# Optimization experiments

Measured on AMD Instinct MI355X. Metric: run time of the kernel, lower is better.

Reference implementation:

```python
import jax, jax.numpy as jnp
import numpy as np

B, T, HW, ENC, DEC, ATT, EMB, V = 32, 128, 14, 2048, 512, 512, 512, 10000
P = HW * HW  # num_pixels = 196


def setup_inputs() -> dict:
    key = jax.random.key(0)
    ks = jax.random.split(key, 24)
    s = 0.02
    inp = {
        'bimgs': jax.random.normal(ks[0], (B, HW, HW, ENC), dtype=jnp.float32),
        'bx': jax.random.randint(ks[1], (B, T), 0, V),
        # torch code assumes lengths sorted DESCENDING
        'bxlen': jnp.sort(jax.random.randint(ks[2], (B,), 1, T + 1))[::-1],
        'emb_W': jax.random.normal(ks[3], (V, EMB)) * s,
        'enc_att_W': jax.random.normal(ks[4], (ATT, ENC)) * s,
        'enc_att_b': jnp.zeros((ATT,)),
        'dec_att_W': jax.random.normal(ks[5], (ATT, DEC)) * s,
        'dec_att_b': jnp.zeros((ATT,)),
        'full_att_W': jax.random.normal(ks[6], (1, ATT)) * s,
        'full_att_b': jnp.zeros((1,)),
        'init_h_W': jax.random.normal(ks[7], (DEC, ENC)) * s,
        'init_h_b': jnp.zeros((DEC,)),
        'init_c_W': jax.random.normal(ks[8], (DEC, ENC)) * s,
        'init_c_b': jnp.zeros((DEC,)),
        'f_beta_W': jax.random.normal(ks[9], (ENC, DEC)) * s,
        'f_beta_b': jnp.zeros((ENC,)),
        'W_ih': jax.random.normal(ks[10], (4 * DEC, EMB + ENC)) * s,
        'b_ih': jnp.zeros((4 * DEC,)),
        'W_hh': jax.random.normal(ks[11], (4 * DEC, DEC)) * s,
        'b_hh': jnp.zeros((4 * DEC,)),
        'fc_W': jax.random.normal(ks[12], (V, DEC)) * s,
        'fc_b': jnp.zeros((V,)),
    }
    return inp


def reference(bimgs, bx, bxlen, emb_W, enc_att_W, enc_att_b, dec_att_W, dec_att_b,
              full_att_W, full_att_b, init_h_W, init_h_b, init_c_W, init_c_b,
              f_beta_W, f_beta_b, W_ih, b_ih, W_hh, b_hh, fc_W, fc_b):
    b = bimgs.shape[0]
    imgs = bimgs.reshape(b, -1, bimgs.shape[-1])          # [B,P,enc]
    t_len = bx.shape[-1]
    embeds = emb_W[bx]                                     # [B,T,E]
    mean_img = imgs.mean(axis=1)                           # [B,enc]
    h0 = mean_img @ init_h_W.T + init_h_b                  # [B,dec]
    c0 = mean_img @ init_c_W.T + init_c_b
    # encoder attention projection is time-invariant -> hoist out of the loop
    att1 = imgs @ enc_att_W.T + enc_att_b                  # [B,P,A]
    active_ts = jnp.arange(t_len)[:, None] < bxlen[None, :]  # [T,B]
    emb_ts = embeds.transpose(1, 0, 2)                     # [T,B,E]

    def step(carry, xs):
        h, c = carry
        emb_t, active = xs
        att2 = h @ dec_att_W.T + dec_att_b                 # [B,A]
        e = jax.nn.relu(att1 + att2[:, None, :]) @ full_att_W[0] + full_att_b[0]  # [B,P]
        alpha = jax.nn.softmax(e, axis=1)
        awe = jnp.einsum('bpe,bp->be', imgs, alpha)        # [B,enc]
        gate = jax.nn.sigmoid(h @ f_beta_W.T + f_beta_b)
        x = jnp.concatenate([emb_t, gate * awe], axis=1)   # [B,E+enc]
        # PyTorch LSTMCell: gate order i, f, g, o
        gates = x @ W_ih.T + b_ih + h @ W_hh.T + b_hh
        i_, f_, g_, o_ = jnp.split(gates, 4, axis=1)
        i_ = jax.nn.sigmoid(i_); f_ = jax.nn.sigmoid(f_); o_ = jax.nn.sigmoid(o_)
        g_ = jnp.tanh(g_)
        c_new = f_ * c + i_ * g_
        h_new = o_ * jnp.tanh(c_new)
        preds = h_new @ fc_W.T + fc_b                      # dropout = identity (eval)
        m = active[:, None]
        h2 = jnp.where(m, h_new, h)
        c2 = jnp.where(m, c_new, c)
        return (h2, c2), (jnp.where(m, preds, 0.0), jnp.where(m, alpha, 0.0))

    _, (preds_ts, alphas_ts) = jax.lax.scan(step, (h0, c0), (emb_ts, active_ts))
    predictions = preds_ts.transpose(1, 0, 2)              # [B,T,V]
    alphas = alphas_ts.transpose(1, 0, 2)                  # [B,T,P]
    return predictions, alphas
```

## Files before the change

### kernel.cpp

```cpp
#include <hip/hip_runtime.h>
#include <hip/hip_bf16.h>

#define BB 32
#define TT 128
#define PP 196
#define ENC 2048
#define DEC 512
#define ATT 512
#define EMB 512
#define VV 10000
#define VVP 10240
#define G4 2048
#define KX 2560

typedef unsigned short u16;
typedef unsigned int u32;
typedef __attribute__((ext_vector_type(8))) short short8;
typedef __attribute__((ext_vector_type(4))) float f32x4;

__device__ __forceinline__ float bf2f(u16 u) { return __uint_as_float(((u32)u) << 16); }
__device__ __forceinline__ u16 f2bf(float f) {
  u32 x = __float_as_uint(f);
  u32 r = (x + 0x7fffu + ((x >> 16) & 1u)) >> 16;
  return (u16)r;
}
__device__ __forceinline__ void unpack8(uint4 v, float* f) {
  f[0] = __uint_as_float(v.x << 16); f[1] = __uint_as_float(v.x & 0xffff0000u);
  f[2] = __uint_as_float(v.y << 16); f[3] = __uint_as_float(v.y & 0xffff0000u);
  f[4] = __uint_as_float(v.z << 16); f[5] = __uint_as_float(v.z & 0xffff0000u);
  f[6] = __uint_as_float(v.w << 16); f[7] = __uint_as_float(v.w & 0xffff0000u);
}
__device__ __forceinline__ void load8(const float* __restrict__ p, float* f) {
  float4 a = ((const float4*)p)[0];
  float4 b = ((const float4*)p)[1];
  f[0] = a.x; f[1] = a.y; f[2] = a.z; f[3] = a.w;
  f[4] = b.x; f[5] = b.y; f[6] = b.z; f[7] = b.w;
}
__device__ __forceinline__ float sigf(float x) { return 1.0f / (1.0f + __expf(-x)); }
__device__ __forceinline__ short8 ld_frag(const u16* __restrict__ p) {
  union { uint4 u; short8 s; } cv;
  cv.u = *(const uint4*)p;
  return cv.s;
}

__global__ __launch_bounds__(256) void k_cvt(const float* __restrict__ src, u16* __restrict__ dst, int n) {
  int i0 = (blockIdx.x * 256 + threadIdx.x) * 8;
  if (i0 >= n) return;
  float f[8]; load8(src + i0, f);
  u16 o[8];
#pragma unroll
  for (int u = 0; u < 8; u++) o[u] = f2bf(f[u]);
  *(uint4*)(dst + i0) = *(const uint4*)o;
}

__global__ __launch_bounds__(256) void k_emball(const int* __restrict__ bx,
    const float* __restrict__ embW, u16* __restrict__ xemb) {
  int flat = blockIdx.x * 256 + threadIdx.x;
  int row = flat >> 6;
  int c8 = (flat & 63) * 8;
  int tok = bx[row];
  const float* e = embW + (size_t)tok * EMB + c8;
  float f[8]; load8(e, f);
  u16 o[8];
#pragma unroll
  for (int u = 0; u < 8; u++) o[u] = f2bf(f[u]);
  *(uint4*)(xemb + (size_t)row * EMB + c8) = *(const uint4*)o;
}

__global__ __launch_bounds__(256) void k_mean(const u16* __restrict__ imgs_bf, u16* __restrict__ mean_bf) {
  int b = blockIdx.x >> 2, chunk = blockIdx.x & 3;
  int ch0 = chunk * 512 + threadIdx.x * 2;
  const u32* base = (const u32*)(imgs_bf + (size_t)b * PP * ENC + ch0);
  float a0 = 0.f, a1 = 0.f;
#pragma unroll 4
  for (int p = 0; p < PP; p++) {
    u32 u = base[(size_t)p * (ENC / 2)];
    a0 += __uint_as_float(u << 16);
    a1 += __uint_as_float(u & 0xffff0000u);
  }
  const float inv = 1.0f / PP;
  u16 o[2] = { f2bf(a0 * inv), f2bf(a1 * inv) };
  *(u32*)(mean_bf + b * ENC + ch0) = *(const u32*)o;
}

__global__ __launch_bounds__(64) void k_init2(const u16* __restrict__ W2_bf,
    const float* __restrict__ ihb, const float* __restrict__ icb,
    const u16* __restrict__ mean_bf, u16* __restrict__ h_bf, float* __restrict__ c) {
  int lane = threadIdx.x;
  int j0 = blockIdx.x * 16;
  int m = lane & 15, quad = lane >> 4;
  const u16* arow = W2_bf + (size_t)(j0 + m) * ENC + quad * 8;
  const u16* xb0 = mean_bf + (size_t)m * ENC + quad * 8;
  const u16* xb1 = mean_bf + (size_t)(16 + m) * ENC + quad * 8;
  f32x4 acc0 = {0.f,0.f,0.f,0.f}, acc1 = {0.f,0.f,0.f,0.f};
  for (int k = 0; k < ENC; k += 32) {
    short8 a = ld_frag(arow + k);
    short8 x0 = ld_frag(xb0 + k);
    short8 x1 = ld_frag(xb1 + k);
    acc0 = __builtin_amdgcn_mfma_f32_16x16x32_bf16(a, x0, acc0, 0, 0, 0);
    acc1 = __builtin_amdgcn_mfma_f32_16x16x32_bf16(a, x1, acc1, 0, 0, 0);
  }
  int jj = j0 + quad * 4;
  int b0 = m, b1 = 16 + m;
#pragma unroll
  for (int r = 0; r < 4; r++) {
    int j = jj + r;
    if (j < 512) {
      float bia = ihb[j];
      h_bf[b0 * DEC + j] = f2bf(acc0[r] + bia);
      h_bf[b1 * DEC + j] = f2bf(acc1[r] + bia);
    } else {
      int g = j - 512;
      float bia = icb[g];
      c[b0 * DEC + g] = acc0[r] + bia;
      c[b1 * DEC + g] = acc1[r] + bia;
    }
  }
}

__global__ __launch_bounds__(256) void k_att1(const u16* __restrict__ imgs_bf,
    const u16* __restrict__ encW_bf, const float* __restrict__ encb, u16* __restrict__ att1) {
  int tid = threadIdx.x;
  int wave = tid >> 6, lane = tid & 63;
  int m0 = blockIdx.x * 32;
  int lm = lane & 15, quad = lane >> 4;
  const u16* b0p = imgs_bf + (size_t)(m0 + lm) * ENC + quad * 8;
  const u16* b1p = imgs_bf + (size_t)(m0 + 16 + lm) * ENC + quad * 8;
  const u16* arow = encW_bf + (size_t)(wave * 128 + lm) * ENC + quad * 8;
  f32x4 acc[8][2];
#pragma unroll
  for (int i = 0; i < 8; i++) { acc[i][0] = (f32x4){0.f,0.f,0.f,0.f}; acc[i][1] = (f32x4){0.f,0.f,0.f,0.f}; }
  for (int k = 0; k < ENC; k += 32) {
    short8 B0 = ld_frag(b0p + k);
    short8 B1 = ld_frag(b1p + k);
#pragma unroll
    for (int i = 0; i < 8; i++) {
      short8 A = ld_frag(arow + (size_t)i * 16 * ENC + k);
      acc[i][0] = __builtin_amdgcn_mfma_f32_16x16x32_bf16(A, B0, acc[i][0], 0, 0, 0);
      acc[i][1] = __builtin_amdgcn_mfma_f32_16x16x32_bf16(A, B1, acc[i][1], 0, 0, 0);
    }
  }
#pragma unroll
  for (int i = 0; i < 8; i++) {
    int jb = wave * 128 + i * 16 + quad * 4;
#pragma unroll
    for (int r = 0; r < 4; r++) {
      int j = jb + r;
      float bia = encb[j];
      att1[(size_t)(m0 + lm) * ATT + j]      = f2bf(acc[i][0][r] + bia);
      att1[(size_t)(m0 + 16 + lm) * ATT + j] = f2bf(acc[i][1][r] + bia);
    }
  }
}

__global__ __launch_bounds__(64) void k_step1(const u16* __restrict__ W3,
    const float* __restrict__ decb, const float* __restrict__ fbb, const float* __restrict__ bhh,
    const u16* __restrict__ h_bf,
    float* __restrict__ att2, float* __restrict__ gate, float* __restrict__ hWhh) {
  int lane = threadIdx.x;
  int j0 = blockIdx.x * 16;
  int m = lane & 15, quad = lane >> 4;
  const u16* arow = W3 + (size_t)(j0 + m) * DEC + quad * 8;
  const u16* xb0 = h_bf + (size_t)m * DEC + quad * 8;
  const u16* xb1 = h_bf + (size_t)(16 + m) * DEC + quad * 8;
  f32x4 acc0 = {0.f,0.f,0.f,0.f}, acc1 = {0.f,0.f,0.f,0.f};
  for (int k = 0; k < DEC; k += 32) {
    short8 a = ld_frag(arow + k);
    short8 x0 = ld_frag(xb0 + k);
    short8 x1 = ld_frag(xb1 + k);
    acc0 = __builtin_amdgcn_mfma_f32_16x16x32_bf16(a, x0, acc0, 0, 0, 0);
    acc1 = __builtin_amdgcn_mfma_f32_16x16x32_bf16(a, x1, acc1, 0, 0, 0);
  }
  int jj = j0 + quad * 4;
  int b0 = m, b1 = 16 + m;
#pragma unroll
  for (int r = 0; r < 4; r++) {
    int j = jj + r;
    float v0 = acc0[r], v1 = acc1[r];
    if (j0 < ATT) {
      float bia = decb[j];
      att2[b0 * ATT + j] = v0 + bia;
      att2[b1 * ATT + j] = v1 + bia;
    } else if (j0 < ATT + ENC) {
      int g = j - ATT;
      float bia = fbb[g];
      gate[b0 * ENC + g] = sigf(v0 + bia);
      gate[b1 * ENC + g] = sigf(v1 + bia);
    } else {
      int g = j - ATT - ENC;
      float bia = bhh[g];
      hWhh[b0 * G4 + g] = v0 + bia;
      hWhh[b1 * G4 + g] = v1 + bia;
    }
  }
}

__global__ __launch_bounds__(256) void k_att(int t, const int* __restrict__ bxlen,
    const u16* __restrict__ att1, const float* __restrict__ att2,
    const float* __restrict__ faW, const float* __restrict__ fab,
    float* __restrict__ alpha_ws, float* __restrict__ out_alphas) {
  int b = blockIdx.x;
  int tid = threadIdx.x;
  if (t >= bxlen[b]) {
    if (tid < PP) out_alphas[((size_t)b * TT + t) * PP + tid] = 0.f;
    return;
  }
  __shared__ float a2[ATT];
  __shared__ float w_s[ATT];
  __shared__ float redw[4], redw2[4];
  for (int i = tid; i < ATT; i += 256) { a2[i] = att2[b * ATT + i]; w_s[i] = faW[i]; }
  __syncthreads();
  float e = -1e30f;
  if (tid < PP) {
    const uint4* ar = (const uint4*)(att1 + (size_t)(b * PP + tid) * ATT);
    float acc = 0.f;
    for (int k = 0; k < ATT; k += 8) {
      float af[8]; unpack8(ar[k >> 3], af);
#pragma unroll
      for (int u = 0; u < 8; u++) {
        float v = af[u] + a2[k + u];
        acc += fmaxf(v, 0.f) * w_s[k + u];
      }
    }
    e = acc + fab[0];
  }
  int lane = tid & 63, wid = tid >> 6;
  float wmax = e;
#pragma unroll
  for (int off = 32; off; off >>= 1) wmax = fmaxf(wmax, __shfl_xor(wmax, off));
  if (lane == 0) redw[wid] = wmax;
  __syncthreads();
  float mx = fmaxf(fmaxf(redw[0], redw[1]), fmaxf(redw[2], redw[3]));
  float ex = (tid < PP) ? __expf(e - mx) : 0.f;
  float wsum = ex;
#pragma unroll
  for (int off = 32; off; off >>= 1) wsum += __shfl_xor(wsum, off);
  if (lane == 0) redw2[wid] = wsum;
  __syncthreads();
  float inv = 1.0f / (redw2[0] + redw2[1] + redw2[2] + redw2[3]);
  if (tid < PP) {
    float al = ex * inv;
    alpha_ws[b * PP + tid] = al;
    out_alphas[((size_t)b * TT + t) * PP + tid] = al;
  }
}

__global__ __launch_bounds__(256) void k_awe(int t, const int* __restrict__ bxlen,
    const u16* __restrict__ imgs_bf, const float* __restrict__ alpha_ws,
    const float* __restrict__ gate, u16* __restrict__ x_awe) {
  int b = blockIdx.x >> 2, chunk = blockIdx.x & 3;
  if (t >= bxlen[b]) return;
  __shared__ float al[PP];
  int tid = threadIdx.x;
  if (tid < PP) al[tid] = alpha_ws[b * PP + tid];
  __syncthreads();
  int ch0 = chunk * 512 + tid * 2;
  const u32* base = (const u32*)(imgs_bf + (size_t)b * PP * ENC + ch0);
  float acc0 = 0.f, acc1 = 0.f;
#pragma unroll 4
  for (int p = 0; p < PP; p++) {
    u32 u = base[(size_t)p * (ENC / 2)];
    float a = al[p];
    acc0 += a * __uint_as_float(u << 16);
    acc1 += a * __uint_as_float(u & 0xffff0000u);
  }
  float2 g = *(const float2*)(gate + b * ENC + ch0);
  u16 o[2] = { f2bf(g.x * acc0), f2bf(g.y * acc1) };
  *(u32*)(x_awe + (size_t)b * ENC + ch0) = *(const u32*)o;
}

__global__ __launch_bounds__(64) void k_gates(int t, const u16* __restrict__ Wih_bf,
    const u16* __restrict__ xemb, const u16* __restrict__ x_awe,
    float* __restrict__ gates_p) {
  int lane = threadIdx.x;
  int j0 = blockIdx.x * 16;
  int y = blockIdx.y;
  int kofs = y * 512;
  int m = lane & 15, quad = lane >> 4;
  const u16* arow = Wih_bf + (size_t)(j0 + m) * KX + kofs + quad * 8;
  const u16 *b0p, *b1p;
  if (y == 0) {
    b0p = xemb + ((size_t)m * TT + t) * EMB + quad * 8;
    b1p = xemb + ((size_t)(16 + m) * TT + t) * EMB + quad * 8;
  } else {
    int ao = kofs - 512;
    b0p = x_awe + (size_t)m * ENC + ao + quad * 8;
    b1p = x_awe + (size_t)(16 + m) * ENC + ao + quad * 8;
  }
  f32x4 acc0 = {0.f,0.f,0.f,0.f}, acc1 = {0.f,0.f,0.f,0.f};
  for (int k = 0; k < 512; k += 32) {
    short8 a = ld_frag(arow + k);
    short8 x0 = ld_frag(b0p + k);
    short8 x1 = ld_frag(b1p + k);
    acc0 = __builtin_amdgcn_mfma_f32_16x16x32_bf16(a, x0, acc0, 0, 0, 0);
    acc1 = __builtin_amdgcn_mfma_f32_16x16x32_bf16(a, x1, acc1, 0, 0, 0);
  }
  float* gp = gates_p + (size_t)y * BB * G4;
  int jj = j0 + quad * 4;
  int b0 = m, b1 = 16 + m;
#pragma unroll
  for (int r = 0; r < 4; r++) {
    int j = jj + r;
    gp[b0 * G4 + j] = acc0[r];
    gp[b1 * G4 + j] = acc1[r];
  }
}

__global__ __launch_bounds__(256) void k_lstm(int t, const int* __restrict__ bxlen,
    const float* __restrict__ gates_p, const float* __restrict__ bih,
    const float* __restrict__ hWhh,
    u16* __restrict__ h_bf, float* __restrict__ c, u16* __restrict__ h_hist) {
  int idx = blockIdx.x * 256 + threadIdx.x;
  int b = idx >> 9, d = idx & 511;
  if (t >= bxlen[b]) return;
  float pre[4];
#pragma unroll
  for (int g = 0; g < 4; g++) {
    int j = g * 512 + d;
    float s = bih[j] + hWhh[b * G4 + j];
#pragma unroll
    for (int cc = 0; cc < 5; cc++) s += gates_p[(size_t)cc * BB * G4 + b * G4 + j];
    pre[g] = s;
  }
  float i_ = sigf(pre[0]);
  float f_ = sigf(pre[1]);
  float g_ = tanhf(pre[2]);
  float o_ = sigf(pre[3]);
  float cn = f_ * c[b * DEC + d] + i_ * g_;
  float hn = o_ * tanhf(cn);
  c[b * DEC + d] = cn;
  u16 hb = f2bf(hn);
  h_bf[b * DEC + d] = hb;
  h_hist[((size_t)b * TT + t) * DEC + d] = hb;
}

__global__ __launch_bounds__(256) void k_fcall(const int* __restrict__ bxlen,
    const u16* __restrict__ fcW_bf, const float* __restrict__ fcb,
    const u16* __restrict__ h_hist, float* __restrict__ preds) {
  int tid = threadIdx.x;
  int wave = tid >> 6, lane = tid & 63;
  int m0 = blockIdx.x * 32;
  int jbase = blockIdx.y * 512 + wave * 128;
  int lm = lane & 15, quad = lane >> 4;
  const u16* b0p = h_hist + (size_t)(m0 + lm) * DEC + quad * 8;
  const u16* b1p = h_hist + (size_t)(m0 + 16 + lm) * DEC + quad * 8;
  const u16* arow = fcW_bf + (size_t)(jbase + lm) * DEC + quad * 8;
  f32x4 acc[8][2];
#pragma unroll
  for (int i = 0; i < 8; i++) { acc[i][0] = (f32x4){0.f,0.f,0.f,0.f}; acc[i][1] = (f32x4){0.f,0.f,0.f,0.f}; }
  for (int k = 0; k < DEC; k += 32) {
    short8 B0 = ld_frag(b0p + k);
    short8 B1 = ld_frag(b1p + k);
#pragma unroll
    for (int i = 0; i < 8; i++) {
      short8 A = ld_frag(arow + (size_t)i * 16 * DEC + k);
      acc[i][0] = __builtin_amdgcn_mfma_f32_16x16x32_bf16(A, B0, acc[i][0], 0, 0, 0);
      acc[i][1] = __builtin_amdgcn_mfma_f32_16x16x32_bf16(A, B1, acc[i][1], 0, 0, 0);
    }
  }
  int row0 = m0 + lm, row1 = m0 + 16 + lm;
  bool act0 = ((row0 & 127) < bxlen[row0 >> 7]);
  bool act1 = ((row1 & 127) < bxlen[row1 >> 7]);
#pragma unroll
  for (int i = 0; i < 8; i++) {
    int jb = jbase + i * 16 + quad * 4;
#pragma unroll
    for (int r = 0; r < 4; r++) {
      int j = jb + r;
      if (j < VV) {
        float bia = fcb[j];
        preds[(size_t)row0 * VV + j] = act0 ? (acc[i][0][r] + bia) : 0.f;
        preds[(size_t)row1 * VV + j] = act1 ? (acc[i][1][r] + bia) : 0.f;
      }
    }
  }
}

extern "C" void kernel_launch(void* const* d_in, const int* in_sizes, int n_in,
                              void* d_out, int out_size, void* d_ws, size_t ws_size,
                              hipStream_t stream) {
  const float* imgs = (const float*)d_in[0];
  const int* bx     = (const int*)d_in[1];
  const int* bxlen  = (const int*)d_in[2];
  const float* embW = (const float*)d_in[3];
  const float* encW = (const float*)d_in[4];
  const float* encb = (const float*)d_in[5];
  const float* decW = (const float*)d_in[6];
  const float* decb = (const float*)d_in[7];
  const float* faW  = (const float*)d_in[8];
  const float* fab  = (const float*)d_in[9];
  const float* ihW  = (const float*)d_in[10];
  const float* ihb  = (const float*)d_in[11];
  const float* icW  = (const float*)d_in[12];
  const float* icb  = (const float*)d_in[13];
  const float* fbW  = (const float*)d_in[14];
  const float* fbb  = (const float*)d_in[15];
  const float* Wih  = (const float*)d_in[16];
  const float* bih  = (const float*)d_in[17];
  const float* Whh  = (const float*)d_in[18];
  const float* bhh  = (const float*)d_in[19];
  const float* fcW  = (const float*)d_in[20];
  const float* fcb  = (const float*)d_in[21];

  float* out_preds  = (float*)d_out;
  float* out_alphas = out_preds + (size_t)BB * TT * VV;

  char* wsb = (char*)d_ws;
  size_t off = 0;
  u16* imgs_bf = (u16*)(wsb + off); off += (size_t)BB * PP * ENC * 2;
  u16* W3_bf   = (u16*)(wsb + off); off += (size_t)4608 * DEC * 2;
  u16* Wih_bf  = (u16*)(wsb + off); off += (size_t)G4 * KX * 2;
  u16* fcW_bf  = (u16*)(wsb + off); off += (size_t)VVP * DEC * 2;
  u16* encW_bf = (u16*)(wsb + off); off += (size_t)ATT * ENC * 2;
  u16* att1    = (u16*)(wsb + off);
  u16* W2_bf   = att1;
  u16* mean_bf = att1 + (size_t)1024 * ENC;
  off += (size_t)BB * PP * ATT * 2;
  u16* xemb    = (u16*)(wsb + off); off += (size_t)BB * TT * EMB * 2;
  u16* h_hist  = (u16*)(wsb + off); off += (size_t)BB * TT * DEC * 2;
  u16* x_awe   = (u16*)(wsb + off); off += (size_t)BB * ENC * 2;
  u16* h_bf    = (u16*)(wsb + off); off += (size_t)BB * DEC * 2;
  float* c      = (float*)(wsb + off); off += (size_t)BB * DEC * 4;
  float* att2   = (float*)(wsb + off); off += (size_t)BB * ATT * 4;
  float* gate   = (float*)(wsb + off); off += (size_t)BB * ENC * 4;
  float* hWhh   = (float*)(wsb + off); off += (size_t)BB * G4 * 4;
  float* gates_p = (float*)(wsb + off); off += (size_t)5 * BB * G4 * 4;
  float* alpha  = (float*)(wsb + off); off += (size_t)BB * PP * 4;

  k_cvt<<<(BB * PP * ENC) / 2048, 256, 0, stream>>>(imgs, imgs_bf, BB * PP * ENC);
  k_cvt<<<(DEC * DEC) / 2048, 256, 0, stream>>>(decW, W3_bf, DEC * DEC);
  k_cvt<<<(ENC * DEC) / 2048, 256, 0, stream>>>(fbW, W3_bf + (size_t)DEC * DEC, ENC * DEC);
  k_cvt<<<(G4 * DEC) / 2048, 256, 0, stream>>>(Whh, W3_bf + (size_t)(DEC + ENC) * DEC, G4 * DEC);
  k_cvt<<<(G4 * KX) / 2048, 256, 0, stream>>>(Wih, Wih_bf, G4 * KX);
  k_cvt<<<(VV * DEC) / 2048, 256, 0, stream>>>(fcW, fcW_bf, VV * DEC);
  k_cvt<<<(ATT * ENC) / 2048, 256, 0, stream>>>(encW, encW_bf, ATT * ENC);
  k_cvt<<<(DEC * ENC) / 2048, 256, 0, stream>>>(ihW, W2_bf, DEC * ENC);
  k_cvt<<<(DEC * ENC) / 2048, 256, 0, stream>>>(icW, W2_bf + (size_t)DEC * ENC, DEC * ENC);
  k_emball<<<(BB * TT * EMB / 8) / 256, 256, 0, stream>>>(bx, embW, xemb);

  k_mean<<<BB * 4, 256, 0, stream>>>(imgs_bf, mean_bf);
  k_init2<<<64, 64, 0, stream>>>(W2_bf, ihb, icb, mean_bf, h_bf, c);
  k_att1<<<(BB * PP) / 32, 256, 0, stream>>>(imgs_bf, encW_bf, encb, att1);

  for (int t = 0; t < TT; t++) {
    k_step1<<<4608 / 16, 64, 0, stream>>>(W3_bf, decb, fbb, bhh, h_bf, att2, gate, hWhh);
    k_att<<<BB, 256, 0, stream>>>(t, bxlen, att1, att2, faW, fab, alpha, out_alphas);
    k_awe<<<BB * 4, 256, 0, stream>>>(t, bxlen, imgs_bf, alpha, gate, x_awe);
    k_gates<<<dim3(G4 / 16, 5), 64, 0, stream>>>(t, Wih_bf, xemb, x_awe, gates_p);
    k_lstm<<<(BB * DEC) / 256, 256, 0, stream>>>(t, bxlen, gates_p, bih, hWhh, h_bf, c, h_hist);
  }
  k_fcall<<<dim3((BB * TT) / 32, 20), 256, 0, stream>>>(bxlen, fcW_bf, fcb, h_hist, out_preds);
}
```

Baseline: 6.286 ms.

## Replace per-step kernel launches with persistent megakernel using grid barriers

Folds the five per-timestep kernels into one persistent kernel of 256 workgroups that loops over all timesteps. Phases are separated by a software grid barrier built on atomics, which removes hundreds of small launches and their gaps. The embedding part of the input-gate GEMM is hoisted out of the loop into a single batched GEMM (k_gemb). The gate GEMM is fused with the LSTM cell update through an in-LDS reduction over an interleaved gate layout. Risks: the kernel relies on all 256 workgroups being co-resident, the barrier spin has a timeout fallback, and there are odd leftover self-assignments including one that touches memory just before alpha_ws.

```diff
diff --git a/kernel.cpp b/kernel.cpp
--- a/kernel.cpp
+++ b/kernel.cpp
@@ -12,6 +12,7 @@
 #define VVP 10240
 #define G4 2048
 #define KX 2560
+#define NWG 256
 
 typedef unsigned short u16;
 typedef unsigned int u32;
@@ -153,185 +154,255 @@
   }
 }
 
-__global__ __launch_bounds__(64) void k_step1(const u16* __restrict__ W3,
-    const float* __restrict__ decb, const float* __restrict__ fbb, const float* __restrict__ bhh,
-    const u16* __restrict__ h_bf,
-    float* __restrict__ att2, float* __restrict__ gate, float* __restrict__ hWhh) {
-  int lane = threadIdx.x;
-  int j0 = blockIdx.x * 16;
-  int m = lane & 15, quad = lane >> 4;
-  const u16* arow = W3 + (size_t)(j0 + m) * DEC + quad * 8;
-  const u16* xb0 = h_bf + (size_t)m * DEC + quad * 8;
-  const u16* xb1 = h_bf + (size_t)(16 + m) * DEC + quad * 8;
-  f32x4 acc0 = {0.f,0.f,0.f,0.f}, acc1 = {0.f,0.f,0.f,0.f};
-  for (int k = 0; k < DEC; k += 32) {
-    short8 a = ld_frag(arow + k);
-    short8 x0 = ld_frag(xb0 + k);
-    short8 x1 = ld_frag(xb1 + k);
-    acc0 = __builtin_amdgcn_mfma_f32_16x16x32_bf16(a, x0, acc0, 0, 0, 0);
-    acc1 = __builtin_amdgcn_mfma_f32_16x16x32_bf16(a, x1, acc1, 0, 0, 0);
-  }
-  int jj = j0 + quad * 4;
-  int b0 = m, b1 = 16 + m;
-#pragma unroll
-  for (int r = 0; r < 4; r++) {
-    int j = jj + r;
-    float v0 = acc0[r], v1 = acc1[r];
-    if (j0 < ATT) {
-      float bia = decb[j];
-      att2[b0 * ATT + j] = v0 + bia;
-      att2[b1 * ATT + j] = v1 + bia;
-    } else if (j0 < ATT + ENC) {
-      int g = j - ATT;
-      float bia = fbb[g];
-      gate[b0 * ENC + g] = sigf(v0 + bia);
-      gate[b1 * ENC + g] = sigf(v1 + bia);
+__global__ __launch_bounds__(256) void k_gemb(const u16* __restrict__ Wih_bf,
+    const u16* __restrict__ xemb, u16* __restrict__ ge) {
+  int tid = threadIdx.x;
+  int wave = tid >> 6, lane = tid & 63;
+  int m0 = blockIdx.x * 32;
+  int jbase = blockIdx.y * 512 + wave * 128;
+  int lm = lane & 15, quad = lane >> 4;
+  const u16* b0p = xemb + ((size_t)(m0 + lm) << 9) + (quad << 3);
+  const u16* b1p = xemb + ((size_t)(m0 + 16 + lm) << 9) + (quad << 3);
+  const u16* arow = Wih_bf + (size_t)(jbase + lm) * KX + (quad << 3);
+  f32x4 acc[8][2];
+#pragma unroll
+  for (int i = 0; i < 8; i++) { acc[i][0] = (f32x4){0.f,0.f,0.f,0.f}; acc[i][1] = (f32x4){0.f,0.f,0.f,0.f}; }
+  for (int k = 0; k < 512; k += 32) {
+    short8 B0 = ld_frag(b0p + k);
+    short8 B1 = ld_frag(b1p + k);
+#pragma unroll
+    for (int i = 0; i < 8; i++) {
+      short8 A = ld_frag(arow + (size_t)i * 16 * KX + k);
+      acc[i][0] = __builtin_amdgcn_mfma_f32_16x16x32_bf16(A, B0, acc[i][0], 0, 0, 0);
+      acc[i][1] = __builtin_amdgcn_mfma_f32_16x16x32_bf16(A, B1, acc[i][1], 0, 0, 0);
+    }
+  }
+#pragma unroll
+  for (int i = 0; i < 8; i++) {
+#pragma unroll
+    for (int r = 0; r < 4; r++) {
+      int j = jbase + i * 16 + quad * 4 + r;
+      int d = j & 511, g9 = j >> 9;
+      int jq = ((d >> 2) << 4) + (g9 << 2) + (d & 3);
+      ge[((size_t)(m0 + lm)) * G4 + jq]      = f2bf(acc[i][0][r]);
+      ge[((size_t)(m0 + 16 + lm)) * G4 + jq] = f2bf(acc[i][1][r]);
+    }
+  }
+}
+
+__global__ void k_zero(unsigned* p) { p[threadIdx.x] = 0u; }
+
+__device__ __forceinline__ void gsync(unsigned* cnt, unsigned* gen) {
+  __syncthreads();
+  if (threadIdx.x == 0) {
+    __threadfence();
+    unsigned g = __hip_atomic_load(gen, __ATOMIC_RELAXED, __HIP_MEMORY_SCOPE_AGENT);
+    unsigned a = __hip_atomic_fetch_add(cnt, 1u, __ATOMIC_RELAXED, __HIP_MEMORY_SCOPE_AGENT);
+    if (a == NWG - 1) {
+      __hip_atomic_store(cnt, 0u, __ATOMIC_RELAXED, __HIP_MEMORY_SCOPE_AGENT);
+      __hip_atomic_store(gen, g + 1u, __ATOMIC_RELEASE, __HIP_MEMORY_SCOPE_AGENT);
     } else {
-      int g = j - ATT - ENC;
-      float bia = bhh[g];
-      hWhh[b0 * G4 + g] = v0 + bia;
-      hWhh[b1 * G4 + g] = v1 + bia;
-    }
-  }
-}
-
-__global__ __launch_bounds__(256) void k_att(int t, const int* __restrict__ bxlen,
-    const u16* __restrict__ att1, const float* __restrict__ att2,
-    const float* __restrict__ faW, const float* __restrict__ fab,
-    float* __restrict__ alpha_ws, float* __restrict__ out_alphas) {
-  int b = blockIdx.x;
-  int tid = threadIdx.x;
-  if (t >= bxlen[b]) {
-    if (tid < PP) out_alphas[((size_t)b * TT + t) * PP + tid] = 0.f;
-    return;
-  }
-  __shared__ float a2[ATT];
-  __shared__ float w_s[ATT];
-  __shared__ float redw[4], redw2[4];
-  for (int i = tid; i < ATT; i += 256) { a2[i] = att2[b * ATT + i]; w_s[i] = faW[i]; }
+      long spins = 0;
+      while (__hip_atomic_load(gen, __ATOMIC_RELAXED, __HIP_MEMORY_SCOPE_AGENT) == g) {
+        __builtin_amdgcn_s_sleep(2);
+        if (++spins > (1L << 26)) break;
+      }
+    }
+    __threadfence();
+  }
   __syncthreads();
-  float e = -1e30f;
-  if (tid < PP) {
-    const uint4* ar = (const uint4*)(att1 + (size_t)(b * PP + tid) * ATT);
-    float acc = 0.f;
-    for (int k = 0; k < ATT; k += 8) {
-      float af[8]; unpack8(ar[k >> 3], af);
-#pragma unroll
-      for (int u = 0; u < 8; u++) {
-        float v = af[u] + a2[k + u];
-        acc += fmaxf(v, 0.f) * w_s[k + u];
-      }
-    }
-    e = acc + fab[0];
-  }
-  int lane = tid & 63, wid = tid >> 6;
-  float wmax = e;
-#pragma unroll
-  for (int off = 32; off; off >>= 1) wmax = fmaxf(wmax, __shfl_xor(wmax, off));
-  if (lane == 0) redw[wid] = wmax;
-  __syncthreads();
-  float mx = fmaxf(fmaxf(redw[0], redw[1]), fmaxf(redw[2], redw[3]));
-  float ex = (tid < PP) ? __expf(e - mx) : 0.f;
-  float wsum = ex;
-#pragma unroll
-  for (int off = 32; off; off >>= 1) wsum += __shfl_xor(wsum, off);
-  if (lane == 0) redw2[wid] = wsum;
-  __syncthreads();
-  float inv = 1.0f / (redw2[0] + redw2[1] + redw2[2] + redw2[3]);
-  if (tid < PP) {
-    float al = ex * inv;
-    alpha_ws[b * PP + tid] = al;
-    out_alphas[((size_t)b * TT + t) * PP + tid] = al;
-  }
-}
-
-__global__ __launch_bounds__(256) void k_awe(int t, const int* __restrict__ bxlen,
-    const u16* __restrict__ imgs_bf, const float* __restrict__ alpha_ws,
-    const float* __restrict__ gate, u16* __restrict__ x_awe) {
-  int b = blockIdx.x >> 2, chunk = blockIdx.x & 3;
-  if (t >= bxlen[b]) return;
-  __shared__ float al[PP];
-  int tid = threadIdx.x;
-  if (tid < PP) al[tid] = alpha_ws[b * PP + tid];
-  __syncthreads();
-  int ch0 = chunk * 512 + tid * 2;
-  const u32* base = (const u32*)(imgs_bf + (size_t)b * PP * ENC + ch0);
-  float acc0 = 0.f, acc1 = 0.f;
+}
+
+__global__ __launch_bounds__(256, 2) void k_mega(
+    const int* __restrict__ bxlen,
+    const u16* __restrict__ W3,
+    const float* __restrict__ decb, const float* __restrict__ fbb,
+    const u16* __restrict__ att1, const float* __restrict__ faW, const float* __restrict__ fab,
+    const u16* __restrict__ imgs_bf, const u16* __restrict__ Wih_bf, const u16* __restrict__ ge,
+    const float* __restrict__ bih, const float* __restrict__ bhh,
+    u16* __restrict__ h_bf, float* __restrict__ c, u16* __restrict__ h_hist,
+    float* __restrict__ att2, float* __restrict__ gatev, float* __restrict__ hWhh,
+    float* __restrict__ alpha_ws, float* __restrict__ out_alphas,
+    unsigned* __restrict__ bar) {
+  const int wg = blockIdx.x;
+  const int tid = threadIdx.x;
+  const int wid = tid >> 6, lane = tid & 63;
+  const int m = lane & 15, quad = lane >> 4;
+  unsigned* cnt = bar;
+  unsigned* gen = bar + 16;
+
+  __shared__ float sA[512], sW[512], sR[4], sR2[4], sAl[PP];
+  __shared__ float sRed[4][16][32];
+
+  if (wg < 32) {
+    for (int i = tid; i < 512; i += 256) sW[i] = faW[i];
+  }
+
+  for (int t = 0; t < TT; t++) {
+    {
+      int gw = (wg << 2) + wid;
+      if (gw < 288) {
+        int j0 = gw << 4;
+        const u16* arow = W3 + ((size_t)(j0 + m) << 9) + (quad << 3);
+        const u16* xb0 = h_bf + ((size_t)m << 9) + (quad << 3);
+        const u16* xb1 = h_bf + ((size_t)(16 + m) << 9) + (quad << 3);
+        f32x4 acc0 = {0.f,0.f,0.f,0.f}, acc1 = {0.f,0.f,0.f,0.f};
 #pragma unroll 4
-  for (int p = 0; p < PP; p++) {
-    u32 u = base[(size_t)p * (ENC / 2)];
-    float a = al[p];
-    acc0 += a * __uint_as_float(u << 16);
-    acc1 += a * __uint_as_float(u & 0xffff0000u);
-  }
-  float2 g = *(const float2*)(gate + b * ENC + ch0);
-  u16 o[2] = { f2bf(g.x * acc0), f2bf(g.y * acc1) };
-  *(u32*)(x_awe + (size_t)b * ENC + ch0) = *(const u32*)o;
-}
-
-__global__ __launch_bounds__(64) void k_gates(int t, const u16* __restrict__ Wih_bf,
-    const u16* __restrict__ xemb, const u16* __restrict__ x_awe,
-    float* __restrict__ gates_p) {
-  int lane = threadIdx.x;
-  int j0 = blockIdx.x * 16;
-  int y = blockIdx.y;
-  int kofs = y * 512;
-  int m = lane & 15, quad = lane >> 4;
-  const u16* arow = Wih_bf + (size_t)(j0 + m) * KX + kofs + quad * 8;
-  const u16 *b0p, *b1p;
-  if (y == 0) {
-    b0p = xemb + ((size_t)m * TT + t) * EMB + quad * 8;
-    b1p = xemb + ((size_t)(16 + m) * TT + t) * EMB + quad * 8;
-  } else {
-    int ao = kofs - 512;
-    b0p = x_awe + (size_t)m * ENC + ao + quad * 8;
-    b1p = x_awe + (size_t)(16 + m) * ENC + ao + quad * 8;
-  }
-  f32x4 acc0 = {0.f,0.f,0.f,0.f}, acc1 = {0.f,0.f,0.f,0.f};
-  for (int k = 0; k < 512; k += 32) {
-    short8 a = ld_frag(arow + k);
-    short8 x0 = ld_frag(b0p + k);
-    short8 x1 = ld_frag(b1p + k);
-    acc0 = __builtin_amdgcn_mfma_f32_16x16x32_bf16(a, x0, acc0, 0, 0, 0);
-    acc1 = __builtin_amdgcn_mfma_f32_16x16x32_bf16(a, x1, acc1, 0, 0, 0);
-  }
-  float* gp = gates_p + (size_t)y * BB * G4;
-  int jj = j0 + quad * 4;
-  int b0 = m, b1 = 16 + m;
-#pragma unroll
-  for (int r = 0; r < 4; r++) {
-    int j = jj + r;
-    gp[b0 * G4 + j] = acc0[r];
-    gp[b1 * G4 + j] = acc1[r];
-  }
-}
-
-__global__ __launch_bounds__(256) void k_lstm(int t, const int* __restrict__ bxlen,
-    const float* __restrict__ gates_p, const float* __restrict__ bih,
-    const float* __restrict__ hWhh,
-    u16* __restrict__ h_bf, float* __restrict__ c, u16* __restrict__ h_hist) {
-  int idx = blockIdx.x * 256 + threadIdx.x;
-  int b = idx >> 9, d = idx & 511;
-  if (t >= bxlen[b]) return;
-  float pre[4];
-#pragma unroll
-  for (int g = 0; g < 4; g++) {
-    int j = g * 512 + d;
-    float s = bih[j] + hWhh[b * G4 + j];
-#pragma unroll
-    for (int cc = 0; cc < 5; cc++) s += gates_p[(size_t)cc * BB * G4 + b * G4 + j];
-    pre[g] = s;
-  }
-  float i_ = sigf(pre[0]);
-  float f_ = sigf(pre[1]);
-  float g_ = tanhf(pre[2]);
-  float o_ = sigf(pre[3]);
-  float cn = f_ * c[b * DEC + d] + i_ * g_;
-  float hn = o_ * tanhf(cn);
-  c[b * DEC + d] = cn;
-  u16 hb = f2bf(hn);
-  h_bf[b * DEC + d] = hb;
-  h_hist[((size_t)b * TT + t) * DEC + d] = hb;
+        for (int k = 0; k < 512; k += 32) {
+          short8 a = ld_frag(arow + k);
+          short8 x0 = ld_frag(xb0 + k);
+          short8 x1 = ld_frag(xb1 + k);
+          acc0 = __builtin_amdgcn_mfma_f32_16x16x32_bf16(a, x0, acc0, 0, 0, 0);
+          acc1 = __builtin_amdgcn_mfma_f32_16x16x32_bf16(a, x1, acc1, 0, 0, 0);
+        }
+        int jj = j0 + (quad << 2);
+        int b0 = m, b1 = 16 + m;
+        if (j0 < 512) {
+#pragma unroll
+          for (int r = 0; r < 4; r++) {
+            int j = jj + r; float bia = decb[j];
+            att2[(b0 << 9) + j] = acc0[r] + bia;
+            att2[(b1 << 9) + j] = acc1[r] + bia;
+          }
+        } else if (j0 < 2560) {
+#pragma unroll
+          for (int r = 0; r < 4; r++) {
+            int g = jj + r - 512; float bia = fbb[g];
+            gatev[(b0 << 11) + g] = sigf(acc0[r] + bia);
+            gatev[(b1 << 11) + g] = sigf(acc1[r] + bia);
+          }
+        } else {
+#pragma unroll
+          for (int r = 0; r < 4; r++) {
+            int j = jj + r - 2560;
+            int d = j & 511, g9 = j >> 9;
+            int jq = ((d >> 2) << 4) + (g9 << 2) + (d & 3);
+            hWhh[(b0 << 11) + jq] = acc0[r];
+            hWhh[(b1 << 11) + jq] = acc1[r];
+          }
+        }
+      }
+    }
+    gsync(cnt, gen);
+
+    if (wg < 32) {
+      int b = wg;
+      if (t < bxlen[b]) {
+        for (int i = tid; i < 512; i += 256) sA[i] = att2[(b << 9) + i];
+        __syncthreads();
+        float e = -1e30f;
+        if (tid < PP) {
+          const uint4* ar = (const uint4*)(att1 + ((size_t)(b * PP + tid) << 9));
+          float acc = 0.f;
+#pragma unroll 4
+          for (int k = 0; k < 512; k += 8) {
+            float af[8]; unpack8(ar[k >> 3], af);
+#pragma unroll
+            for (int u = 0; u < 8; u++) {
+              float v = af[u] + sA[k + u];
+              acc += fmaxf(v, 0.f) * sW[k + u];
+            }
+          }
+          e = acc + fab[0];
+        }
+        float wmax = e;
+#pragma unroll
+        for (int off = 32; off; off >>= 1) wmax = fmaxf(wmax, __shfl_xor(wmax, off));
+        if (lane == 0) sR[wid] = wmax;
+        __syncthreads();
+        float mx = fmaxf(fmaxf(sR[0], sR[1]), fmaxf(sR[2], sR[3]));
+        float ex = (tid < PP) ? __expf(e - mx) : 0.f;
+        float wsum = ex;
+#pragma unroll
+        for (int off = 32; off; off >>= 1) wsum += __shfl_xor(wsum, off);
+        if (lane == 0) sR2[wid] = wsum;
+        __syncthreads();
+        float inv = 1.0f / (sR2[0] + sR2[1] + sR2[2] + sR2[3]);
+        if (tid < PP) {
+          float al = ex * inv;
+          alpha_ws[b * PP + tid] = al;
+          out_alphas[((size_t)b * TT + t) * PP + tid] = al;
+        }
+      } else {
+        if (tid < PP) out_alphas[((size_t)b * TT + t) * PP + tid] = 0.f;
+      }
+    }
+    gsync(cnt, gen);
+
+    {
+      int b = wg >> 3;
+      int ch = ((wg & 7) << 8) + tid;
+      if (tid < PP) sAl[tid] = alpha_ws[b * PP + tid];
+      __syncthreads();
+      const u16* base = imgs_bf + (((size_t)b * PP) << 11) + ch;
+      float acc = 0.f;
+#pragma unroll 4
+      for (int p = 0; p < PP; p++) acc += sAl[p] * bf2f(base[(size_t)p << 11]);
+      ((u16*)att2)[0] = ((u16*)att2)[0];
+      {
+        extern __device__ u16 __dummy_unused;
+      }
+      u16 v = f2bf(gatev[(b << 11) + ch] * acc);
+      ((u16*)alpha_ws)[-1] = ((u16*)alpha_ws)[-1];
+      x_awe_store:;
+      ((u16*)(hWhh + (BB * G4)))[ (b << 11) + ch ] = v;
+    }
+    gsync(cnt, gen);
+
+    if (wg < 128) {
+      const u16* x_awe = (const u16*)(hWhh + (BB * G4));
+      int q = wg;
+      int k0 = (wid << 9);
+      int jm = ((m >> 2) << 9) + (q << 2) + (m & 3);
+      const u16* arow = Wih_bf + (size_t)jm * KX + 512 + k0 + (quad << 3);
+      const u16* xb0 = x_awe + ((size_t)m << 11) + k0 + (quad << 3);
+      const u16* xb1 = x_awe + ((size_t)(16 + m) << 11) + k0 + (quad << 3);
+      f32x4 acc0 = {0.f,0.f,0.f,0.f}, acc1 = {0.f,0.f,0.f,0.f};
+#pragma unroll 4
+      for (int k = 0; k < 512; k += 32) {
+        short8 a = ld_frag(arow + k);
+        short8 x0 = ld_frag(xb0 + k);
+        short8 x1 = ld_frag(xb1 + k);
+        acc0 = __builtin_amdgcn_mfma_f32_16x16x32_bf16(a, x0, acc0, 0, 0, 0);
+        acc1 = __builtin_amdgcn_mfma_f32_16x16x32_bf16(a, x1, acc1, 0, 0, 0);
+      }
+#pragma unroll
+      for (int r = 0; r < 4; r++) {
+        int jl = (quad << 2) + r;
+        sRed[wid][jl][m] = acc0[r];
+        sRed[wid][jl][16 + m] = acc1[r];
+      }
+      __syncthreads();
+      if (tid < 128) {
+        int b = tid & 31, r = tid >> 5;
+        if (t < bxlen[b]) {
+          int d = (q << 2) + r;
+          float pre[4];
+#pragma unroll
+          for (int g = 0; g < 4; g++) {
+            int jl = (g << 2) + r;
+            int j = (g << 9) + d;
+            int jq = (q << 4) + jl;
+            float s = sRed[0][jl][b] + sRed[1][jl][b] + sRed[2][jl][b] + sRed[3][jl][b];
+            s += bf2f(ge[((size_t)b * TT + t) * G4 + jq]);
+            s += hWhh[(b << 11) + jq] + bih[j] + bhh[j];
+            pre[g] = s;
+          }
+          float i_ = sigf(pre[0]);
+          float f_ = sigf(pre[1]);
+          float g_ = tanhf(pre[2]);
+          float o_ = sigf(pre[3]);
+          float cn = f_ * c[(b << 9) + d] + i_ * g_;
+          float hn = o_ * tanhf(cn);
+          c[(b << 9) + d] = cn;
+          u16 hb = f2bf(hn);
+          h_bf[(b << 9) + d] = hb;
+          h_hist[((size_t)b * TT + t) * DEC + d] = hb;
+        }
+      }
+    }
+    gsync(cnt, gen);
+  }
 }
 
 __global__ __launch_bounds__(256) void k_fcall(const int* __restrict__ bxlen,
@@ -418,14 +489,16 @@
   off += (size_t)BB * PP * ATT * 2;
   u16* xemb    = (u16*)(wsb + off); off += (size_t)BB * TT * EMB * 2;
   u16* h_hist  = (u16*)(wsb + off); off += (size_t)BB * TT * DEC * 2;
-  u16* x_awe   = (u16*)(wsb + off); off += (size_t)BB * ENC * 2;
+  u16* ge      = (u16*)(wsb + off); off += (size_t)BB * TT * G4 * 2;
   u16* h_bf    = (u16*)(wsb + off); off += (size_t)BB * DEC * 2;
   float* c      = (float*)(wsb + off); off += (size_t)BB * DEC * 4;
   float* att2   = (float*)(wsb + off); off += (size_t)BB * ATT * 4;
-  float* gate   = (float*)(wsb + off); off += (size_t)BB * ENC * 4;
+  float* gatev  = (float*)(wsb + off); off += (size_t)BB * ENC * 4;
   float* hWhh   = (float*)(wsb + off); off += (size_t)BB * G4 * 4;
-  float* gates_p = (float*)(wsb + off); off += (size_t)5 * BB * G4 * 4;
+  u16* x_awe    = (u16*)(wsb + off); off += (size_t)BB * ENC * 2;
   float* alpha  = (float*)(wsb + off); off += (size_t)BB * PP * 4;
+  unsigned* bar = (unsigned*)(wsb + off); off += 256;
+  (void)x_awe;
 
   k_cvt<<<(BB * PP * ENC) / 2048, 256, 0, stream>>>(imgs, imgs_bf, BB * PP * ENC);
   k_cvt<<<(DEC * DEC) / 2048, 256, 0, stream>>>(decW, W3_bf, DEC * DEC);
@@ -437,17 +510,17 @@
   k_cvt<<<(DEC * ENC) / 2048, 256, 0, stream>>>(ihW, W2_bf, DEC * ENC);
   k_cvt<<<(DEC * ENC) / 2048, 256, 0, stream>>>(icW, W2_bf + (size_t)DEC * ENC, DEC * ENC);
   k_emball<<<(BB * TT * EMB / 8) / 256, 256, 0, stream>>>(bx, embW, xemb);
+  k_gemb<<<dim3((BB * TT) / 32, 4), 256, 0, stream>>>(Wih_bf, xemb, ge);
 
   k_mean<<<BB * 4, 256, 0, stream>>>(imgs_bf, mean_bf);
   k_init2<<<64, 64, 0, stream>>>(W2_bf, ihb, icb, mean_bf, h_bf, c);
   k_att1<<<(BB * PP) / 32, 256, 0, stream>>>(imgs_bf, encW_bf, encb, att1);
-
-  for (int t = 0; t < TT; t++) {
-    k_step1<<<4608 / 16, 64, 0, stream>>>(W3_bf, decb, fbb, bhh, h_bf, att2, gate, hWhh);
-    k_att<<<BB, 256, 0, stream>>>(t, bxlen, att1, att2, faW, fab, alpha, out_alphas);
-    k_awe<<<BB * 4, 256, 0, stream>>>(t, bxlen, imgs_bf, alpha, gate, x_awe);
-    k_gates<<<dim3(G4 / 16, 5), 64, 0, stream>>>(t, Wih_bf, xemb, x_awe, gates_p);
-    k_lstm<<<(BB * DEC) / 256, 256, 0, stream>>>(t, bxlen, gates_p, bih, hWhh, h_bf, c, h_hist);
-  }
+  k_zero<<<1, 64, 0, stream>>>(bar);
+
+  k_mega<<<NWG, 256, 0, stream>>>(bxlen, W3_bf, decb, fbb, att1, faW, fab,
+                                  imgs_bf, Wih_bf, ge, bih, bhh,
+                                  h_bf, c, h_hist, att2, gatev, hWhh,
+                                  alpha, out_alphas, bar);
+
   k_fcall<<<dim3((BB * TT) / 32, 20), 256, 0, stream>>>(bxlen, fcW_bf, fcb, h_hist, out_preds);
 }
```

Result: slower. 18.36 ms (+192.1%).
